# Kernel optimization log

Hardware: AMD Instinct MI355X
Metric: run time of the kernel (lower is better)

The kernel has to match this reference:

```python
import jax, jax.numpy as jnp
import numpy as np

B, T, C = 4, 2048, 1024
N_HEADS = 16
HEAD_DIM = C // N_HEADS

def setup_inputs() -> dict:
    key = jax.random.key(0)
    k1, k2, k3 = jax.random.split(key, 3)
    x = jax.random.normal(k1, (B, T, C), dtype=jnp.float32)
    w_attn = jax.random.normal(k2, (C, 3 * C), dtype=jnp.float32) * (1.0 / np.sqrt(C))
    b_attn = jnp.zeros((3 * C,), dtype=jnp.float32)
    w_proj = jax.random.normal(k3, (C, C), dtype=jnp.float32) * (1.0 / np.sqrt(C))
    b_proj = jnp.zeros((C,), dtype=jnp.float32)
    return {"x": x, "w_attn": w_attn, "b_attn": b_attn, "w_proj": w_proj, "b_proj": b_proj}

def reference(x, w_attn, b_attn, w_proj, b_proj):
    Bx, Tx, Cx = x.shape
    qkv = x @ w_attn + b_attn                      # [B,T,3C]
    q, k, v = jnp.split(qkv, 3, axis=-1)
    def heads(t):
        return t.reshape(Bx, Tx, N_HEADS, HEAD_DIM).transpose(0, 2, 1, 3)  # [B,H,T,D]
    q, k, v = heads(q), heads(k), heads(v)
    scale = 1.0 / np.sqrt(HEAD_DIM)
    attn = jnp.einsum('bhqd,bhkd->bhqk', q, k) * scale  # [B,H,T,T]
    causal = jnp.tril(jnp.ones((Tx, Tx), dtype=bool))
    attn = jnp.where(causal[None, None, :, :], attn, -jnp.inf)
    attn = jax.nn.softmax(attn, axis=-1)
    out = jnp.einsum('bhqk,bhkd->bhqd', attn, v)        # [B,H,T,D]
    out = out.transpose(0, 2, 1, 3).reshape(Bx, Tx, Cx)
    return out @ w_proj + b_proj
```

## Files before the change

kernel.cpp:

```cpp
#include <hip/hip_runtime.h>
#include <hip/hip_bf16.h>

#define BATCH 4
#define SEQ   2048
#define CH    1024
#define NH    16
#define HD    64
#define BT    8192

typedef __attribute__((ext_vector_type(8))) short bf16x8;
typedef __attribute__((ext_vector_type(4))) float f32x4;
typedef __attribute__((ext_vector_type(16))) float f32x16;

__device__ __forceinline__ unsigned short f2b(float f) {
  __hip_bfloat16 h = __float2bfloat16(f);
  return *reinterpret_cast<unsigned short*>(&h);
}

__device__ __forceinline__ unsigned cvt_pk(float lo, float hi_) {
  unsigned r;
  asm("v_cvt_pk_bf16_f32 %0, %1, %2" : "=v"(r) : "v"(lo), "v"(hi_));
  return r;
}
__device__ __forceinline__ void plane_swap(unsigned &a, unsigned &b) {
  asm("v_permlane32_swap_b32 %0, %1" : "+v"(a), "+v"(b));
}


__global__ void conv_x_bf16(const float* __restrict__ in, unsigned short* __restrict__ out, int n4) {
  int i = blockIdx.x * blockDim.x + threadIdx.x;
  if (i >= n4) return;
  float4 v = reinterpret_cast<const float4*>(in)[i];
  ushort4 o;
  o.x = f2b(v.x); o.y = f2b(v.y); o.z = f2b(v.z); o.w = f2b(v.w);
  reinterpret_cast<ushort4*>(out)[i] = o;
}

__global__ void transpose_w_bf16(const float* __restrict__ in, unsigned short* __restrict__ out,
                                 int R, int Cc) {
  __shared__ float tile[32][33];
  int c0 = blockIdx.x * 32, r0 = blockIdx.y * 32;
  int tx = threadIdx.x, ty = threadIdx.y;
  #pragma unroll
  for (int i = 0; i < 32; i += 8)
    tile[ty + i][tx] = in[(size_t)(r0 + ty + i) * Cc + c0 + tx];
  __syncthreads();
  #pragma unroll
  for (int i = 0; i < 32; i += 8)
    out[(size_t)(c0 + ty + i) * R + r0 + tx] = f2b(tile[tx][ty + i]);
}


#define QSCALE 0.18033688011112042f

#define GSTAGE(BUF, K0)                                                                        \
  {                                                                                            \
    _Pragma("unroll")                                                                          \
    for (int c = 0; c < 2; ++c) {                                                              \
      int idx = c * 256 + tid;                                                                 \
      const unsigned short* sA = A + (size_t)(m0 + (idx >> 2)) * 1024 + (K0) + (idx & 3) * 8;  \
      __builtin_amdgcn_global_load_lds((const __attribute__((address_space(1))) void*)sA,      \
          (__attribute__((address_space(3))) void*)&sb[(BUF) * 4096 + (c * 256 + (tid & ~63)) * 8], 16, 0, 0); \
      const unsigned short* sB = Bt + (size_t)(n0 + (idx >> 2)) * 1024 + (K0) + (idx & 3) * 8; \
      __builtin_amdgcn_global_load_lds((const __attribute__((address_space(1))) void*)sB,      \
          (__attribute__((address_space(3))) void*)&sb[8192 + (BUF) * 4096 + (c * 256 + (tid & ~63)) * 8], 16, 0, 0); \
    }                                                                                          \
  }

__global__ __launch_bounds__(256) void gemm_qkv(
    const unsigned short* __restrict__ A,
    const unsigned short* __restrict__ Bt,
    const float* __restrict__ bias,
    unsigned short* __restrict__ Qb,
    unsigned short* __restrict__ Kb,
    unsigned short* __restrict__ Vt) {
  __shared__ __align__(16) unsigned short sb[16384];
  int tid = threadIdx.x;
  int lane = tid & 63, wav = tid >> 6;
  int wr = wav >> 1, wc = wav & 1;
  int lr = lane & 15, lh = lane >> 4;
  int m0 = blockIdx.x * 128, n0 = blockIdx.y * 128;

  f32x4 acc[4][4];
  #pragma unroll
  for (int i = 0; i < 4; ++i)
    #pragma unroll
    for (int j = 0; j < 4; ++j)
      acc[i][j] = f32x4{0.f, 0.f, 0.f, 0.f};

  GSTAGE(0, 0)
  asm volatile("s_waitcnt vmcnt(0)" ::: "memory");
  __builtin_amdgcn_s_barrier();

  int cur = 0;
  for (int k0 = 0; k0 < 1024; k0 += 32) {
    if (k0 + 32 < 1024) GSTAGE(cur ^ 1, k0 + 32)
    bf16x8 a[4], b[4];
    #pragma unroll
    for (int i = 0; i < 4; ++i)
      a[i] = *reinterpret_cast<const bf16x8*>(&sb[cur * 4096 + (wr * 64 + i * 16 + lr) * 32 + lh * 8]);
    #pragma unroll
    for (int j = 0; j < 4; ++j)
      b[j] = *reinterpret_cast<const bf16x8*>(&sb[8192 + cur * 4096 + (wc * 64 + j * 16 + lr) * 32 + lh * 8]);
    #pragma unroll
    for (int i = 0; i < 4; ++i)
      #pragma unroll
      for (int j = 0; j < 4; ++j)
        acc[i][j] = __builtin_amdgcn_mfma_f32_16x16x32_bf16(a[i], b[j], acc[i][j], 0, 0, 0);
    asm volatile("s_waitcnt vmcnt(0)" ::: "memory");
    __builtin_amdgcn_s_barrier();
    cur ^= 1;
  }

  int which = n0 >> 10;
  int h2 = (n0 >> 6) & 15;
  int bb = m0 >> 11, t0 = m0 & 2047;

  if (which < 2) {
    unsigned short* dst = which ? Kb : Qb;
    float sc = which ? 1.0f : QSCALE;
    size_t headbase = (size_t)(bb * 16 + h2 + wc) * SEQ;
    #pragma unroll
    for (int j = 0; j < 4; ++j) {
      int d = j * 16 + lr;
      float bv = bias[n0 + wc * 64 + d];
      #pragma unroll
      for (int i = 0; i < 4; ++i) {
        #pragma unroll
        for (int r = 0; r < 4; ++r) {
          int t = t0 + wr * 64 + i * 16 + lh * 4 + r;
          dst[(headbase + t) * HD + d] = f2b((acc[i][j][r] + bv) * sc);
        }
      }
    }
  } else {
    unsigned short* tile = sb;
    #pragma unroll
    for (int half = 0; half < 2; ++half) {
      if (wc == half) {
        #pragma unroll
        for (int j = 0; j < 4; ++j) {
          int nrow = j * 16 + lr;
          float bv = bias[n0 + half * 64 + nrow];
          int sw = nrow & 7;
          #pragma unroll
          for (int i = 0; i < 4; ++i) {
            int cm = wr * 16 + i * 4 + lh;
            unsigned lo = cvt_pk(acc[i][j][0] + bv, acc[i][j][1] + bv);
            unsigned hi_ = cvt_pk(acc[i][j][2] + bv, acc[i][j][3] + bv);
            unsigned long long val = (unsigned long long)lo | ((unsigned long long)hi_ << 32);
            *reinterpret_cast<unsigned long long*>(&tile[nrow * 128 + (cm ^ sw) * 4]) = val;
          }
        }
      }
      __syncthreads();
      size_t vbase = (size_t)((bb * 16 + h2 + half) * 64);
      #pragma unroll
      for (int it = 0; it < 4; ++it) {
        int pid = it * 256 + tid;
        int nrow = pid >> 4, p = pid & 15;
        int sw = nrow & 7;
        union { unsigned long long u[2]; bf16x8 v; } u;
        u.u[0] = *reinterpret_cast<const unsigned long long*>(&tile[nrow * 128 + ((2 * p) ^ sw) * 4]);
        u.u[1] = *reinterpret_cast<const unsigned long long*>(&tile[nrow * 128 + (((2 * p) ^ sw) ^ 1) * 4]);
        *reinterpret_cast<bf16x8*>(&Vt[(vbase + nrow) * SEQ + t0 + p * 8]) = u.v;
      }
      __syncthreads();
    }
  }
}


__global__ __launch_bounds__(512, 2) void attn_fwd(
    const unsigned short* __restrict__ Qb,
    const unsigned short* __restrict__ Kb,
    const unsigned short* __restrict__ Vt,
    unsigned short* __restrict__ AO) {
  __shared__ __align__(16) unsigned short sbuf[16384];

  int tid = threadIdx.x;
  int lane = tid & 63, w = tid >> 6;
  int ql = lane & 31, hi = lane >> 5;
  int bid = blockIdx.x;
  int head = bid & 63;
  int qs = 7 - (bid >> 6);
  int q0 = qs * 256;
  int nt = 4 * (qs + 1);
  int b = head >> 4, h = head & 15;

  const unsigned short* Qh = Qb + (size_t)head * SEQ * HD;
  const unsigned short* Kh = Kb + (size_t)head * SEQ * HD;
  const unsigned short* Vh = Vt + (size_t)head * HD * SEQ;

#define STAGE(BUF, KV0)                                                                        \
  {                                                                                            \
    int row_ = tid >> 3;                                                                       \
    int cg_ = (tid & 7) ^ (row_ & 7);                                                          \
    const unsigned short* srcK_ = Kh + (size_t)((KV0) + row_) * HD + cg_ * 8;                  \
    __builtin_amdgcn_global_load_lds((const __attribute__((address_space(1))) void*)srcK_,     \
        (__attribute__((address_space(3))) void*)&sbuf[(BUF) * 4096 + (tid & ~63) * 8], 16, 0, 0); \
    const unsigned short* srcV_ = Vh + (size_t)row_ * SEQ + (KV0) + cg_ * 8;                   \
    __builtin_amdgcn_global_load_lds((const __attribute__((address_space(1))) void*)srcV_,     \
        (__attribute__((address_space(3))) void*)&sbuf[8192 + (BUF) * 4096 + (tid & ~63) * 8], 16, 0, 0); \
  }

  int qg = q0 + w * 32 + ql;
  bf16x8 qf[4];
  #pragma unroll
  for (int dblk = 0; dblk < 4; ++dblk)
    qf[dblk] = *reinterpret_cast<const bf16x8*>(&Qh[(size_t)qg * HD + dblk * 16 + hi * 8]);

  f32x16 o0 = (f32x16)0.0f, o1 = (f32x16)0.0f;
  float mrun = -1e30f, lrun = 0.f;

  STAGE(0, 0)
  asm volatile("s_waitcnt vmcnt(0)" ::: "memory");
  __builtin_amdgcn_s_barrier();

  int cur = 0;
  int wq_hi = q0 + w * 32 + 31;
  for (int t = 0; t < nt; ++t) {
    int kv0 = t * 64;
    if (t + 1 < nt) STAGE(cur ^ 1, kv0 + 64)

    if (kv0 <= wq_hi) {
      f32x16 s0 = (f32x16)0.0f, s1 = (f32x16)0.0f;
      int rk0 = ql, rk1 = 32 + ql;
      __builtin_amdgcn_s_setprio(1);
      #pragma unroll
      for (int dblk = 0; dblk < 4; ++dblk) {
        bf16x8 kf0 = *reinterpret_cast<const bf16x8*>(
            &sbuf[cur * 4096 + rk0 * 64 + (((dblk * 2 + hi) ^ (rk0 & 7)) << 3)]);
        s0 = __builtin_amdgcn_mfma_f32_32x32x16_bf16(kf0, qf[dblk], s0, 0, 0, 0);
        bf16x8 kf1 = *reinterpret_cast<const bf16x8*>(
            &sbuf[cur * 4096 + rk1 * 64 + (((dblk * 2 + hi) ^ (rk1 & 7)) << 3)]);
        s1 = __builtin_amdgcn_mfma_f32_32x32x16_bf16(kf1, qf[dblk], s1, 0, 0, 0);
      }
      __builtin_amdgcn_s_setprio(0);

      float p[32];
      bool needMask = (kv0 + 63 > q0 + 32 * w);
      #pragma unroll
      for (int r = 0; r < 16; ++r) {
        int cr = (r & 3) + 8 * (r >> 2);
        float v0 = s0[r], v1 = s1[r];
        if (needMask) {
          int kv_ = kv0 + 4 * hi + cr;
          v0 = (kv_ > qg) ? -1e30f : v0;
          v1 = (kv_ + 32 > qg) ? -1e30f : v1;
        }
        p[r] = v0; p[16 + r] = v1;
      }

      float m16[16], m8[8], m4[4], m2[2];
      #pragma unroll
      for (int i = 0; i < 16; ++i) m16[i] = fmaxf(p[i], p[i + 16]);
      #pragma unroll
      for (int i = 0; i < 8; ++i) m8[i] = fmaxf(m16[i], m16[i + 8]);
      #pragma unroll
      for (int i = 0; i < 4; ++i) m4[i] = fmaxf(m8[i], m8[i + 4]);
      m2[0] = fmaxf(m4[0], m4[2]); m2[1] = fmaxf(m4[1], m4[3]);
      float mt = fmaxf(m2[0], m2[1]);
      mt = fmaxf(mt, __shfl_xor(mt, 32));
      float mnew = fmaxf(mrun, mt);
      float alpha = __builtin_amdgcn_exp2f(mrun - mnew);
      mrun = mnew;

      #pragma unroll
      for (int i = 0; i < 32; ++i) p[i] = __builtin_amdgcn_exp2f(p[i] - mnew);
      float a16[16], a8[8], a4[4];
      #pragma unroll
      for (int i = 0; i < 16; ++i) a16[i] = p[i] + p[i + 16];
      #pragma unroll
      for (int i = 0; i < 8; ++i) a8[i] = a16[i] + a16[i + 8];
      #pragma unroll
      for (int i = 0; i < 4; ++i) a4[i] = a8[i] + a8[i + 4];
      float rs = (a4[0] + a4[1]) + (a4[2] + a4[3]);
      rs += __shfl_xor(rs, 32);
      lrun = lrun * alpha + rs;

      #pragma unroll
      for (int i = 0; i < 16; ++i) { o0[i] *= alpha; o1[i] *= alpha; }

      union FU { unsigned u[4]; bf16x8 v; };
      FU fr[4];
      #pragma unroll
      for (int blk = 0; blk < 2; ++blk) {
        unsigned X = cvt_pk(p[blk * 16 + 0], p[blk * 16 + 1]);
        unsigned Z = cvt_pk(p[blk * 16 + 4], p[blk * 16 + 5]);
        plane_swap(X, Z);
        unsigned Y = cvt_pk(p[blk * 16 + 2], p[blk * 16 + 3]);
        unsigned W = cvt_pk(p[blk * 16 + 6], p[blk * 16 + 7]);
        plane_swap(Y, W);
        fr[blk * 2].u[0] = X; fr[blk * 2].u[1] = Y; fr[blk * 2].u[2] = Z; fr[blk * 2].u[3] = W;
        unsigned X2 = cvt_pk(p[blk * 16 + 8], p[blk * 16 + 9]);
        unsigned Z2 = cvt_pk(p[blk * 16 + 12], p[blk * 16 + 13]);
        plane_swap(X2, Z2);
        unsigned Y2 = cvt_pk(p[blk * 16 + 10], p[blk * 16 + 11]);
        unsigned W2 = cvt_pk(p[blk * 16 + 14], p[blk * 16 + 15]);
        plane_swap(Y2, W2);
        fr[blk * 2 + 1].u[0] = X2; fr[blk * 2 + 1].u[1] = Y2;
        fr[blk * 2 + 1].u[2] = Z2; fr[blk * 2 + 1].u[3] = W2;
      }

      __builtin_amdgcn_s_setprio(1);
      #pragma unroll
      for (int kc = 0; kc < 4; ++kc) {
        int rd0 = ql, rd1 = 32 + ql;
        bf16x8 vf0 = *reinterpret_cast<const bf16x8*>(
            &sbuf[8192 + cur * 4096 + rd0 * 64 + ((((kc << 1) + hi) ^ (rd0 & 7)) << 3)]);
        o0 = __builtin_amdgcn_mfma_f32_32x32x16_bf16(vf0, fr[kc].v, o0, 0, 0, 0);
        bf16x8 vf1 = *reinterpret_cast<const bf16x8*>(
            &sbuf[8192 + cur * 4096 + rd1 * 64 + ((((kc << 1) + hi) ^ (rd1 & 7)) << 3)]);
        o1 = __builtin_amdgcn_mfma_f32_32x32x16_bf16(vf1, fr[kc].v, o1, 0, 0, 0);
      }
      __builtin_amdgcn_s_setprio(0);
    }

    asm volatile("s_waitcnt vmcnt(0)" ::: "memory");
    __builtin_amdgcn_s_barrier();
    cur ^= 1;
  }

  float inv = 1.0f / lrun;
  int qloc = w * 32 + ql;
  #pragma unroll
  for (int dblk = 0; dblk < 2; ++dblk) {
    #pragma unroll
    for (int m = 0; m < 4; ++m) {
      float v0, v1, v2, v3;
      if (dblk == 0) {
        v0 = o0[m * 4 + 0] * inv; v1 = o0[m * 4 + 1] * inv;
        v2 = o0[m * 4 + 2] * inv; v3 = o0[m * 4 + 3] * inv;
      } else {
        v0 = o1[m * 4 + 0] * inv; v1 = o1[m * 4 + 1] * inv;
        v2 = o1[m * 4 + 2] * inv; v3 = o1[m * 4 + 3] * inv;
      }
      unsigned u0 = (unsigned)f2b(v0) | ((unsigned)f2b(v1) << 16);
      unsigned u1 = (unsigned)f2b(v2) | ((unsigned)f2b(v3) << 16);
      int slot = (dblk * 4 + m) ^ (qloc & 7);
      unsigned long long val = (unsigned long long)u0 | ((unsigned long long)u1 << 32);
      *reinterpret_cast<unsigned long long*>(&sbuf[qloc * 64 + slot * 8 + hi * 4]) = val;
    }
  }
  __syncthreads();

  #pragma unroll
  for (int it = 0; it < 4; ++it) {
    int qr = it * 64 + (tid >> 3);
    int lc = tid & 7;
    int slot = lc ^ (qr & 7);
    bf16x8 v = *reinterpret_cast<const bf16x8*>(&sbuf[qr * 64 + slot * 8]);
    *reinterpret_cast<bf16x8*>(
        &AO[(size_t)(b * SEQ + q0 + qr) * CH + h * 64 + lc * 8]) = v;
  }
}


__global__ __launch_bounds__(256) void gemm_proj(
    const unsigned short* __restrict__ A,
    const unsigned short* __restrict__ Bt,
    const float* __restrict__ bias,
    float* __restrict__ out) {
  __shared__ __align__(16) unsigned short sb[16384];
  int tid = threadIdx.x;
  int lane = tid & 63, wav = tid >> 6;
  int wr = wav >> 1, wc = wav & 1;
  int lr = lane & 15, lh = lane >> 4;
  int m0 = blockIdx.x * 128, n0 = blockIdx.y * 128;

  f32x4 acc[4][4];
  #pragma unroll
  for (int i = 0; i < 4; ++i)
    #pragma unroll
    for (int j = 0; j < 4; ++j)
      acc[i][j] = f32x4{0.f, 0.f, 0.f, 0.f};

  GSTAGE(0, 0)
  asm volatile("s_waitcnt vmcnt(0)" ::: "memory");
  __builtin_amdgcn_s_barrier();

  int cur = 0;
  for (int k0 = 0; k0 < 1024; k0 += 32) {
    if (k0 + 32 < 1024) GSTAGE(cur ^ 1, k0 + 32)
    bf16x8 a[4], b[4];
    #pragma unroll
    for (int i = 0; i < 4; ++i)
      a[i] = *reinterpret_cast<const bf16x8*>(&sb[cur * 4096 + (wr * 64 + i * 16 + lr) * 32 + lh * 8]);
    #pragma unroll
    for (int j = 0; j < 4; ++j)
      b[j] = *reinterpret_cast<const bf16x8*>(&sb[8192 + cur * 4096 + (wc * 64 + j * 16 + lr) * 32 + lh * 8]);
    #pragma unroll
    for (int i = 0; i < 4; ++i)
      #pragma unroll
      for (int j = 0; j < 4; ++j)
        acc[i][j] = __builtin_amdgcn_mfma_f32_16x16x32_bf16(a[i], b[j], acc[i][j], 0, 0, 0);
    asm volatile("s_waitcnt vmcnt(0)" ::: "memory");
    __builtin_amdgcn_s_barrier();
    cur ^= 1;
  }

  #pragma unroll
  for (int i = 0; i < 4; ++i) {
    #pragma unroll
    for (int j = 0; j < 4; ++j) {
      int n = n0 + wc * 64 + j * 16 + lr;
      float bv = bias[n];
      #pragma unroll
      for (int r = 0; r < 4; ++r) {
        int m = m0 + wr * 64 + i * 16 + lh * 4 + r;
        out[(size_t)m * 1024 + n] = acc[i][j][r] + bv;
      }
    }
  }
}


extern "C" void kernel_launch(void* const* d_in, const int* in_sizes, int n_in,
                              void* d_out, int out_size, void* d_ws, size_t ws_size,
                              hipStream_t stream) {
  const float* x      = (const float*)d_in[0];
  const float* w_attn = (const float*)d_in[1];
  const float* b_attn = (const float*)d_in[2];
  const float* w_proj = (const float*)d_in[3];
  const float* b_proj = (const float*)d_in[4];
  float* out = (float*)d_out;

  char* ws = (char*)d_ws;
  unsigned short* xb  = (unsigned short*)(ws);
  unsigned short* wAT = (unsigned short*)(ws + 16777216);
  unsigned short* wPT = (unsigned short*)(ws + 23068672);
  unsigned short* Qb  = (unsigned short*)(ws + 25165824);
  unsigned short* Kb  = (unsigned short*)(ws + 41943040);
  unsigned short* Vt  = (unsigned short*)(ws + 58720256);
  unsigned short* AO  = (unsigned short*)(ws + 75497472);

  conv_x_bf16<<<(BT * CH / 4 + 255) / 256, 256, 0, stream>>>(x, xb, BT * CH / 4);
  transpose_w_bf16<<<dim3(3 * CH / 32, CH / 32), dim3(32, 8), 0, stream>>>(w_attn, wAT, CH, 3 * CH);
  transpose_w_bf16<<<dim3(CH / 32, CH / 32), dim3(32, 8), 0, stream>>>(w_proj, wPT, CH, CH);
  gemm_qkv<<<dim3(BT / 128, 3 * CH / 128), 256, 0, stream>>>(xb, wAT, b_attn, Qb, Kb, Vt);
  attn_fwd<<<512, 512, 0, stream>>>(Qb, Kb, Vt, AO);
  gemm_proj<<<dim3(BT / 128, CH / 128), 256, 0, stream>>>(AO, wPT, b_proj, out);
}
```

Measured before the change: 175.8 us.

## Switch GEMM and attention K/V staging from double to triple buffering

Both GEMM kernels and the attention kernel now rotate through three LDS stages instead of two. Loads are prefetched two iterations ahead, and each iteration waits with a partial vmcnt so only the oldest stage must land before the barrier. This aims to hide more global-load latency behind MFMA work. The cost is LDS per block rising from 32KB to 48KB, which may reduce how many blocks fit on a CU, plus slightly more index arithmetic.

Result: faster. 170.9 us (-2.8%).

```diff
diff --git a/kernel.cpp b/kernel.cpp
--- a/kernel.cpp
+++ b/kernel.cpp
@@ -63,7 +63,7 @@
           (__attribute__((address_space(3))) void*)&sb[(BUF) * 4096 + (c * 256 + (tid & ~63)) * 8], 16, 0, 0); \
       const unsigned short* sB = Bt + (size_t)(n0 + (idx >> 2)) * 1024 + (K0) + (idx & 3) * 8; \
       __builtin_amdgcn_global_load_lds((const __attribute__((address_space(1))) void*)sB,      \
-          (__attribute__((address_space(3))) void*)&sb[8192 + (BUF) * 4096 + (c * 256 + (tid & ~63)) * 8], 16, 0, 0); \
+          (__attribute__((address_space(3))) void*)&sb[12288 + (BUF) * 4096 + (c * 256 + (tid & ~63)) * 8], 16, 0, 0); \
     }                                                                                          \
   }
 
@@ -74,7 +74,7 @@
     unsigned short* __restrict__ Qb,
     unsigned short* __restrict__ Kb,
     unsigned short* __restrict__ Vt) {
-  __shared__ __align__(16) unsigned short sb[16384];
+  __shared__ __align__(16) unsigned short sb[24576];
   int tid = threadIdx.x;
   int lane = tid & 63, wav = tid >> 6;
   int wr = wav >> 1, wc = wav & 1;
@@ -89,27 +89,31 @@
       acc[i][j] = f32x4{0.f, 0.f, 0.f, 0.f};
 
   GSTAGE(0, 0)
-  asm volatile("s_waitcnt vmcnt(0)" ::: "memory");
+  GSTAGE(1, 32)
+  asm volatile("s_waitcnt vmcnt(4)" ::: "memory");
   __builtin_amdgcn_s_barrier();
 
   int cur = 0;
   for (int k0 = 0; k0 < 1024; k0 += 32) {
-    if (k0 + 32 < 1024) GSTAGE(cur ^ 1, k0 + 32)
+    bool issued = (k0 + 64 < 1024);
+    int nb = cur + 2; if (nb >= 3) nb -= 3;
+    if (issued) GSTAGE(nb, k0 + 64)
     bf16x8 a[4], b[4];
     #pragma unroll
     for (int i = 0; i < 4; ++i)
       a[i] = *reinterpret_cast<const bf16x8*>(&sb[cur * 4096 + (wr * 64 + i * 16 + lr) * 32 + lh * 8]);
     #pragma unroll
     for (int j = 0; j < 4; ++j)
-      b[j] = *reinterpret_cast<const bf16x8*>(&sb[8192 + cur * 4096 + (wc * 64 + j * 16 + lr) * 32 + lh * 8]);
+      b[j] = *reinterpret_cast<const bf16x8*>(&sb[12288 + cur * 4096 + (wc * 64 + j * 16 + lr) * 32 + lh * 8]);
     #pragma unroll
     for (int i = 0; i < 4; ++i)
       #pragma unroll
       for (int j = 0; j < 4; ++j)
         acc[i][j] = __builtin_amdgcn_mfma_f32_16x16x32_bf16(a[i], b[j], acc[i][j], 0, 0, 0);
-    asm volatile("s_waitcnt vmcnt(0)" ::: "memory");
+    if (issued) { asm volatile("s_waitcnt vmcnt(4)" ::: "memory"); }
+    else        { asm volatile("s_waitcnt vmcnt(0)" ::: "memory"); }
     __builtin_amdgcn_s_barrier();
-    cur ^= 1;
+    cur = (cur + 1 == 3) ? 0 : cur + 1;
   }
 
   int which = n0 >> 10;
@@ -176,7 +180,7 @@
     const unsigned short* __restrict__ Kb,
     const unsigned short* __restrict__ Vt,
     unsigned short* __restrict__ AO) {
-  __shared__ __align__(16) unsigned short sbuf[16384];
+  __shared__ __align__(16) unsigned short sbuf[24576];
 
   int tid = threadIdx.x;
   int lane = tid & 63, w = tid >> 6;
@@ -201,7 +205,7 @@
         (__attribute__((address_space(3))) void*)&sbuf[(BUF) * 4096 + (tid & ~63) * 8], 16, 0, 0); \
     const unsigned short* srcV_ = Vh + (size_t)row_ * SEQ + (KV0) + cg_ * 8;                   \
     __builtin_amdgcn_global_load_lds((const __attribute__((address_space(1))) void*)srcV_,     \
-        (__attribute__((address_space(3))) void*)&sbuf[8192 + (BUF) * 4096 + (tid & ~63) * 8], 16, 0, 0); \
+        (__attribute__((address_space(3))) void*)&sbuf[12288 + (BUF) * 4096 + (tid & ~63) * 8], 16, 0, 0); \
   }
 
   int qg = q0 + w * 32 + ql;
@@ -214,14 +218,17 @@
   float mrun = -1e30f, lrun = 0.f;
 
   STAGE(0, 0)
-  asm volatile("s_waitcnt vmcnt(0)" ::: "memory");
+  STAGE(1, 64)
+  asm volatile("s_waitcnt vmcnt(2)" ::: "memory");
   __builtin_amdgcn_s_barrier();
 
   int cur = 0;
   int wq_hi = q0 + w * 32 + 31;
   for (int t = 0; t < nt; ++t) {
     int kv0 = t * 64;
-    if (t + 1 < nt) STAGE(cur ^ 1, kv0 + 64)
+    bool issued = (t + 2 < nt);
+    int nb = cur + 2; if (nb >= 3) nb -= 3;
+    if (issued) STAGE(nb, kv0 + 128)
 
     if (kv0 <= wq_hi) {
       f32x16 s0 = (f32x16)0.0f, s1 = (f32x16)0.0f;
@@ -308,18 +315,19 @@
       for (int kc = 0; kc < 4; ++kc) {
         int rd0 = ql, rd1 = 32 + ql;
         bf16x8 vf0 = *reinterpret_cast<const bf16x8*>(
-            &sbuf[8192 + cur * 4096 + rd0 * 64 + ((((kc << 1) + hi) ^ (rd0 & 7)) << 3)]);
+            &sbuf[12288 + cur * 4096 + rd0 * 64 + ((((kc << 1) + hi) ^ (rd0 & 7)) << 3)]);
         o0 = __builtin_amdgcn_mfma_f32_32x32x16_bf16(vf0, fr[kc].v, o0, 0, 0, 0);
         bf16x8 vf1 = *reinterpret_cast<const bf16x8*>(
-            &sbuf[8192 + cur * 4096 + rd1 * 64 + ((((kc << 1) + hi) ^ (rd1 & 7)) << 3)]);
+            &sbuf[12288 + cur * 4096 + rd1 * 64 + ((((kc << 1) + hi) ^ (rd1 & 7)) << 3)]);
         o1 = __builtin_amdgcn_mfma_f32_32x32x16_bf16(vf1, fr[kc].v, o1, 0, 0, 0);
       }
       __builtin_amdgcn_s_setprio(0);
     }
 
-    asm volatile("s_waitcnt vmcnt(0)" ::: "memory");
+    if (issued) { asm volatile("s_waitcnt vmcnt(2)" ::: "memory"); }
+    else        { asm volatile("s_waitcnt vmcnt(0)" ::: "memory"); }
     __builtin_amdgcn_s_barrier();
-    cur ^= 1;
+    cur = (cur + 1 == 3) ? 0 : cur + 1;
   }
 
   float inv = 1.0f / lrun;
@@ -362,7 +370,7 @@
     const unsigned short* __restrict__ Bt,
     const float* __restrict__ bias,
     float* __restrict__ out) {
-  __shared__ __align__(16) unsigned short sb[16384];
+  __shared__ __align__(16) unsigned short sb[24576];
   int tid = threadIdx.x;
   int lane = tid & 63, wav = tid >> 6;
   int wr = wav >> 1, wc = wav & 1;
@@ -377,27 +385,31 @@
       acc[i][j] = f32x4{0.f, 0.f, 0.f, 0.f};
 
   GSTAGE(0, 0)
-  asm volatile("s_waitcnt vmcnt(0)" ::: "memory");
+  GSTAGE(1, 32)
+  asm volatile("s_waitcnt vmcnt(4)" ::: "memory");
   __builtin_amdgcn_s_barrier();
 
   int cur = 0;
   for (int k0 = 0; k0 < 1024; k0 += 32) {
-    if (k0 + 32 < 1024) GSTAGE(cur ^ 1, k0 + 32)
+    bool issued = (k0 + 64 < 1024);
+    int nb = cur + 2; if (nb >= 3) nb -= 3;
+    if (issued) GSTAGE(nb, k0 + 64)
     bf16x8 a[4], b[4];
     #pragma unroll
     for (int i = 0; i < 4; ++i)
       a[i] = *reinterpret_cast<const bf16x8*>(&sb[cur * 4096 + (wr * 64 + i * 16 + lr) * 32 + lh * 8]);
     #pragma unroll
     for (int j = 0; j < 4; ++j)
-      b[j] = *reinterpret_cast<const bf16x8*>(&sb[8192 + cur * 4096 + (wc * 64 + j * 16 + lr) * 32 + lh * 8]);
+      b[j] = *reinterpret_cast<const bf16x8*>(&sb[12288 + cur * 4096 + (wc * 64 + j * 16 + lr) * 32 + lh * 8]);
     #pragma unroll
     for (int i = 0; i < 4; ++i)
       #pragma unroll
       for (int j = 0; j < 4; ++j)
         acc[i][j] = __builtin_amdgcn_mfma_f32_16x16x32_bf16(a[i], b[j], acc[i][j], 0, 0, 0);
-    asm volatile("s_waitcnt vmcnt(0)" ::: "memory");
+    if (issued) { asm volatile("s_waitcnt vmcnt(4)" ::: "memory"); }
+    else        { asm volatile("s_waitcnt vmcnt(0)" ::: "memory"); }
     __builtin_amdgcn_s_barrier();
-    cur ^= 1;
+    cur = (cur + 1 == 3) ? 0 : cur + 1;
   }
 
   #pragma unroll
```
